# Optimization experiments

Measured on AMD Instinct MI355X. Metric: run time of the kernel, lower is better.

## Reference

```python
import jax, jax.numpy as jnp
import numpy as np

EPS = 1e-5
NUM_LAYERS = 3


def _batchnorm(h, g, b):
    mean = h.mean(axis=0)
    var = h.var(axis=0)  # biased variance, matches torch BatchNorm training math
    return (h - mean) * jax.lax.rsqrt(var + EPS) * g + b


def setup_inputs() -> dict:
    key = jax.random.key(0)
    ks = jax.random.split(key, 8)
    N, E, D, H, OUT = 100000, 1600000, 128, 128, 64
    s = 0.08  # weight scale for numerical sanity
    return {
        "x": jax.random.normal(ks[0], (N, D), jnp.float32),
        "edge_index": jax.random.randint(ks[1], (2, E), 0, N, jnp.int64),
        "Wl": jax.random.normal(ks[2], (NUM_LAYERS, D, H), jnp.float32) * s,
        "bl": jnp.zeros((NUM_LAYERS, H), jnp.float32),
        "Wr": jax.random.normal(ks[3], (NUM_LAYERS, D, H), jnp.float32) * s,
        "gamma": jnp.ones((NUM_LAYERS, H), jnp.float32),
        "beta": jnp.zeros((NUM_LAYERS, H), jnp.float32),
        "W1": jax.random.normal(ks[4], (D + NUM_LAYERS * H, 2 * OUT), jnp.float32) * s,
        "b1": jnp.zeros((2 * OUT,), jnp.float32),
        "g1": jnp.ones((2 * OUT,), jnp.float32),
        "be1": jnp.zeros((2 * OUT,), jnp.float32),
        "W2": jax.random.normal(ks[5], (2 * OUT, OUT), jnp.float32) * s,
        "b2": jnp.zeros((OUT,), jnp.float32),
    }


def reference(x, edge_index, Wl, bl, Wr, gamma, beta, W1, b1, g1, be1, W2, b2):
    # GraphSAGE: stacked SAGEConv(mean aggr) + BatchNorm + ReLU, JK-concat, 2-layer MLP head.
    # Dropout is identity (eval mode).
    N = x.shape[0]
    src, dst = edge_index[0], edge_index[1]
    deg = jax.ops.segment_sum(jnp.ones((src.shape[0],), x.dtype), dst, num_segments=N)
    inv_deg = (1.0 / jnp.maximum(deg, 1.0))[:, None]  # [N,1]
    xs = [x]
    h = x
    for i in range(NUM_LAYERS):
        # mean-aggregate neighbor features, then linear (same math as PyG SAGEConv)
        agg = jax.ops.segment_sum(h[src], dst, num_segments=N) * inv_deg  # [N,D]
        h = agg @ Wl[i] + bl[i] + h @ Wr[i]
        h = _batchnorm(h, gamma[i], beta[i])
        h = jax.nn.relu(h)
        xs.append(h)
    z = jnp.concatenate(xs, axis=-1)  # [N, D + L*H]
    z = _batchnorm(z @ W1 + b1, g1, be1)
    z = jax.nn.leaky_relu(z, negative_slope=0.01)
    return z @ W2 + b2
```

## Files before the change

kernel.cpp:

```cpp
#include <hip/hip_runtime.h>
#include <hip/hip_bf16.h>

#define CDIV(a,b) (((a)+(b)-1)/(b))

typedef __attribute__((ext_vector_type(8))) short short8_t;
typedef __attribute__((ext_vector_type(4))) float f32x4;

__device__ __forceinline__ float b2f(ushort u){
    union { uint i; float f; } v; v.i = ((uint)u) << 16; return v.f;
}
__device__ __forceinline__ ushort f2b(float f){
    __hip_bfloat16 h = __float2bfloat16(f);
    return *reinterpret_cast<ushort*>(&h);
}


__global__ __launch_bounds__(256) void k_bcount(
    const int* __restrict__ dst, int E, int nbuck, int* __restrict__ bcnt)
{
    __shared__ int cnt[512];
    const int t = threadIdx.x;
    for (int i = t; i < nbuck; i += 256) cnt[i] = 0;
    __syncthreads();
    const int e0 = blockIdx.x * 4096;
    #pragma unroll
    for (int q = 0; q < 16; ++q){
        int idx = e0 + q*256 + t;
        if (idx < E) atomicAdd(&cnt[dst[idx] >> 8], 1);
    }
    __syncthreads();
    for (int i = t; i < nbuck; i += 256){
        int c = cnt[i];
        if (c) atomicAdd(&bcnt[i], c);
    }
}

__global__ void k_bscan(const int* __restrict__ bcnt, int nbuck, int E,
                        int* __restrict__ bbase, int* __restrict__ gcur)
{
    __shared__ int s[512];
    int t = threadIdx.x;
    int v = (t < nbuck) ? bcnt[t] : 0;
    s[t] = v;
    __syncthreads();
    for (int off = 1; off < 512; off <<= 1){
        int x = (t >= off) ? s[t-off] : 0;
        __syncthreads();
        s[t] += x;
        __syncthreads();
    }
    if (t < nbuck){ int e = s[t] - v; bbase[t] = e; gcur[t] = e; }
    if (t == 0) bbase[nbuck] = E;
}

__global__ __launch_bounds__(256) void k_bucketA(
    const int* __restrict__ src, const int* __restrict__ dst, int E,
    int nbuck, int* __restrict__ gcur, uint* __restrict__ ebuf)
{
    __shared__ int cnt[512];
    __shared__ int base[512];
    const int t  = threadIdx.x;
    const int e0 = blockIdx.x * 4096;
    for (int i = t; i < nbuck; i += 256) cnt[i] = 0;
    __syncthreads();
    uint pk[16]; int mb[16];
    #pragma unroll
    for (int q = 0; q < 16; ++q){
        int idx = e0 + q*256 + t;
        int b = -1; uint pkv = 0;
        if (idx < E){
            int s = src[idx], d = dst[idx];
            b = d >> 8;
            pkv = (uint)s | ((uint)(d & 255) << 24);
            atomicAdd(&cnt[b], 1);
        }
        mb[q] = b; pk[q] = pkv;
    }
    __syncthreads();
    for (int i = t; i < nbuck; i += 256){
        int c = cnt[i];
        base[i] = c ? atomicAdd(&gcur[i], c) : 0;
    }
    __syncthreads();
    for (int i = t; i < nbuck; i += 256) cnt[i] = 0;
    __syncthreads();
    #pragma unroll
    for (int q = 0; q < 16; ++q){
        if (mb[q] >= 0){
            int b   = mb[q];
            int pos = base[b] + atomicAdd(&cnt[b], 1);
            ebuf[pos] = pk[q];
        }
    }
}

__global__ __launch_bounds__(256) void k_build(
    const uint* __restrict__ ebuf, const int* __restrict__ bbase,
    int N, int E, int* __restrict__ row_ptr, float* __restrict__ inv_deg,
    int* __restrict__ col_idx)
{
    __shared__ int cnt[256];
    __shared__ int scn[256];
    const int b = blockIdx.x;
    const int t = threadIdx.x;
    const int n0 = b << 8;
    const int ebase = bbase[b], eend = bbase[b+1];

    cnt[t] = 0;
    __syncthreads();
    for (int j = ebase + t; j < eend; j += 256)
        atomicAdd(&cnt[ebuf[j] >> 24], 1);
    __syncthreads();

    int d = cnt[t];
    scn[t] = d;
    __syncthreads();
    for (int off = 1; off < 256; off <<= 1){
        int x = (t >= off) ? scn[t-off] : 0;
        __syncthreads();
        scn[t] += x;
        __syncthreads();
    }
    int excl = scn[t] - d;
    int node = n0 + t;
    if (node < N){
        row_ptr[node] = ebase + excl;
        inv_deg[node] = 1.0f / (float)(d > 1 ? d : 1);
    }
    if (b == 0 && t == 0) row_ptr[N] = E;

    cnt[t] = excl;
    __syncthreads();
    for (int j = ebase + t; j < eend; j += 256){
        uint e = ebuf[j];
        int p = atomicAdd(&cnt[e >> 24], 1);
        col_idx[ebase + p] = (int)(e & 0xFFFFFFu);
    }
}

__global__ void k_cvt_x(const float* __restrict__ in, ushort* __restrict__ out, int n4){
    int i = blockIdx.x*blockDim.x + threadIdx.x;
    if (i >= n4) return;
    float4 v = reinterpret_cast<const float4*>(in)[i];
    ushort4 o; o.x=f2b(v.x); o.y=f2b(v.y); o.z=f2b(v.z); o.w=f2b(v.w);
    reinterpret_cast<ushort4*>(out)[i] = o;
}

__global__ void k_cvt_t(const float* __restrict__ in, ushort* __restrict__ out,
                        int K, int C, int total){
    int i = blockIdx.x*blockDim.x + threadIdx.x;
    if (i >= total) return;
    int kc = K*C;
    int s = i / kc, r = i - s*kc;
    int k = r / C, c = r - k*C;
    out[s*kc + c*K + k] = f2b(in[i]);
}

__global__ __launch_bounds__(256) void k_agg_bf(
    const ushort* __restrict__ h, const int* __restrict__ row_ptr,
    const int* __restrict__ col_idx, const float* __restrict__ inv_deg,
    ushort* __restrict__ agg, int N)
{
    int node = (blockIdx.x*blockDim.x + threadIdx.x) >> 6;
    int lane = threadIdx.x & 63;
    if (node >= N) return;
    const int g = lane >> 4, l15 = lane & 15;
    const int beg = row_ptr[node], end = row_ptr[node+1];

    float a[8];
    #pragma unroll
    for (int q = 0; q < 8; ++q) a[q] = 0.f;

    int j = beg + g;
    while (j + 4 < end){
        int s0 = col_idx[j];
        int s1 = col_idx[j+4];
        uint4 v0 = *reinterpret_cast<const uint4*>(h + (size_t)s0*128 + l15*8);
        uint4 v1 = *reinterpret_cast<const uint4*>(h + (size_t)s1*128 + l15*8);
        uint w0[4] = {v0.x, v0.y, v0.z, v0.w};
        uint w1[4] = {v1.x, v1.y, v1.z, v1.w};
        #pragma unroll
        for (int q = 0; q < 4; ++q){
            a[2*q]   += b2f((ushort)(w0[q] & 0xffffu)) + b2f((ushort)(w1[q] & 0xffffu));
            a[2*q+1] += b2f((ushort)(w0[q] >> 16))     + b2f((ushort)(w1[q] >> 16));
        }
        j += 8;
    }
    if (j < end){
        int s0 = col_idx[j];
        uint4 v0 = *reinterpret_cast<const uint4*>(h + (size_t)s0*128 + l15*8);
        uint w0[4] = {v0.x, v0.y, v0.z, v0.w};
        #pragma unroll
        for (int q = 0; q < 4; ++q){
            a[2*q]   += b2f((ushort)(w0[q] & 0xffffu));
            a[2*q+1] += b2f((ushort)(w0[q] >> 16));
        }
    }

    #pragma unroll
    for (int q = 0; q < 8; ++q){
        a[q] += __shfl_xor(a[q], 16);
        a[q] += __shfl_xor(a[q], 32);
    }

    if (g == 0){
        float sc = inv_deg[node];
        uint r[4];
        #pragma unroll
        for (int q = 0; q < 4; ++q)
            r[q] = (uint)f2b(a[2*q]*sc) | ((uint)f2b(a[2*q+1]*sc) << 16);
        *reinterpret_cast<uint4*>(agg + (size_t)node*128 + l15*8) =
            make_uint4(r[0], r[1], r[2], r[3]);
    }
}

template<int NCF, int STATS, int OUTBF>
__global__ __launch_bounds__(256) void k_gemm_mfma(
    const ushort* __restrict__ A0, const ushort* __restrict__ T0,
    const ushort* __restrict__ A1, const ushort* __restrict__ T1,
    const ushort* __restrict__ A2, const ushort* __restrict__ T2,
    const ushort* __restrict__ A3, const ushort* __restrict__ T3,
    int P, const float* __restrict__ bias,
    ushort* __restrict__ out_bf, float* __restrict__ out_f32,
    float* __restrict__ partials, int N)
{
    __shared__ ushort Ws[NCF*16*128];
    const int t   = threadIdx.x;
    const int w   = t >> 6, l = t & 63;
    const int l15 = l & 15, lg = l >> 4;
    const int r0   = blockIdx.x * 128;
    const int wrow = w * 32;

    f32x4 acc[2][NCF];
    #pragma unroll
    for (int i = 0; i < 2; ++i)
        #pragma unroll
        for (int j = 0; j < NCF; ++j) acc[i][j] = (f32x4){0.f,0.f,0.f,0.f};

    for (int p = 0; p < P; ++p){
        const ushort* A = (p==0)?A0:(p==1)?A1:(p==2)?A2:A3;
        const ushort* T = (p==0)?T0:(p==1)?T1:(p==2)?T2:T3;
        if (p) __syncthreads();
        #pragma unroll
        for (int q = 0; q < NCF; ++q){
            int lin  = q*256 + t;
            int row  = lin >> 4, c16 = lin & 15;
            int c16s = c16 ^ (row & 7);
            uint4 v = *reinterpret_cast<const uint4*>(T + (size_t)row*128 + c16*8);
            *reinterpret_cast<uint4*>(&Ws[row*128 + c16s*8]) = v;
        }
        __syncthreads();
        #pragma unroll
        for (int kk = 0; kk < 4; ++kk){
            const int k0 = kk*32;
            short8_t a[2];
            #pragma unroll
            for (int rf = 0; rf < 2; ++rf){
                size_t gr = (size_t)(r0 + wrow + rf*16 + l15);
                a[rf] = *reinterpret_cast<const short8_t*>(A + gr*128 + k0 + lg*8);
            }
            #pragma unroll
            for (int cf = 0; cf < NCF; ++cf){
                int row  = cf*16 + l15;
                int c16  = (k0 >> 3) + lg;
                int c16s = c16 ^ (row & 7);
                short8_t b = *reinterpret_cast<const short8_t*>(&Ws[row*128 + c16s*8]);
                acc[0][cf] = __builtin_amdgcn_mfma_f32_16x16x32_bf16(a[0], b, acc[0][cf], 0, 0, 0);
                acc[1][cf] = __builtin_amdgcn_mfma_f32_16x16x32_bf16(a[1], b, acc[1][cf], 0, 0, 0);
            }
        }
    }

    float bs[NCF];
    #pragma unroll
    for (int cf = 0; cf < NCF; ++cf) bs[cf] = bias[cf*16 + l15];

    float s1[NCF], s2[NCF];
    #pragma unroll
    for (int cf = 0; cf < NCF; ++cf){ s1[cf] = 0.f; s2[cf] = 0.f; }

    #pragma unroll
    for (int rf = 0; rf < 2; ++rf){
        #pragma unroll
        for (int q = 0; q < 4; ++q){
            int gr = r0 + wrow + rf*16 + lg*4 + q;
            bool valid = gr < N;
            #pragma unroll
            for (int cf = 0; cf < NCF; ++cf){
                float v = acc[rf][cf][q] + bs[cf];
                if (valid){
                    if (STATS){ s1[cf] += v; s2[cf] += v*v; }
                    int col = cf*16 + l15;
                    if (OUTBF) out_bf[(size_t)gr*(NCF*16) + col] = f2b(v);
                    else       out_f32[(size_t)gr*(NCF*16) + col] = v;
                }
            }
        }
    }
    if (STATS){
        #pragma unroll
        for (int cf = 0; cf < NCF; ++cf){
            s1[cf] += __shfl_xor(s1[cf], 16);
            s1[cf] += __shfl_xor(s1[cf], 32);
            s2[cf] += __shfl_xor(s2[cf], 16);
            s2[cf] += __shfl_xor(s2[cf], 32);
        }
        if (l < 16){
            float* pb = partials + (size_t)(blockIdx.x*4 + w)*256;
            #pragma unroll
            for (int cf = 0; cf < NCF; ++cf){
                pb[cf*16 + l15]       = s1[cf];
                pb[128 + cf*16 + l15] = s2[cf];
            }
        }
    }
}

__global__ void k_bnreduce(const float* __restrict__ partials, int I, int N,
                           const float* __restrict__ gamma, const float* __restrict__ beta,
                           float* __restrict__ ss)
{
    int c = blockIdx.x;
    int l = threadIdx.x;
    float s1 = 0.f, s2 = 0.f;
    for (int i = l; i < I; i += 64){
        s1 += partials[(size_t)i*256 + c];
        s2 += partials[(size_t)i*256 + 128 + c];
    }
    #pragma unroll
    for (int off = 32; off; off >>= 1){
        s1 += __shfl_xor(s1, off);
        s2 += __shfl_xor(s2, off);
    }
    if (l == 0){
        float m   = s1 / (float)N;
        float var = s2 / (float)N - m*m;
        float sc  = rsqrtf(var + 1e-5f) * gamma[c];
        ss[c]     = sc;
        ss[128+c] = beta[c] - m*sc;
    }
}

template<int LEAKY>
__global__ __launch_bounds__(256) void k_norm_act_bf(
    const ushort* __restrict__ pre, const float* __restrict__ ss,
    ushort* __restrict__ out, int total8)
{
    int i = blockIdx.x*blockDim.x + threadIdx.x;
    if (i >= total8) return;
    uint4 v = reinterpret_cast<const uint4*>(pre)[i];
    int c0 = (i & 15) * 8;
    uint vv[4] = {v.x, v.y, v.z, v.w};
    uint r[4];
    #pragma unroll
    for (int q = 0; q < 4; ++q){
        float f0 = b2f((ushort)(vv[q] & 0xffffu)) * ss[c0+q*2]   + ss[128+c0+q*2];
        float f1 = b2f((ushort)(vv[q] >> 16))     * ss[c0+q*2+1] + ss[128+c0+q*2+1];
        if (LEAKY){ f0 = f0 > 0.f ? f0 : 0.01f*f0; f1 = f1 > 0.f ? f1 : 0.01f*f1; }
        else      { f0 = fmaxf(f0, 0.f); f1 = fmaxf(f1, 0.f); }
        r[q] = (uint)f2b(f0) | ((uint)f2b(f1) << 16);
    }
    reinterpret_cast<uint4*>(out)[i] = make_uint4(r[0], r[1], r[2], r[3]);
}

extern "C" void kernel_launch(void* const* d_in, const int* in_sizes, int n_in,
                              void* d_out, int out_size, void* d_ws, size_t ws_size,
                              hipStream_t stream)
{
    const float* x     = (const float*)d_in[0];
    const int*   ei    = (const int*)  d_in[1];
    const float* Wl    = (const float*)d_in[2];
    const float* bl    = (const float*)d_in[3];
    const float* Wr    = (const float*)d_in[4];
    const float* gamma = (const float*)d_in[5];
    const float* beta  = (const float*)d_in[6];
    const float* W1    = (const float*)d_in[7];
    const float* b1    = (const float*)d_in[8];
    const float* g1    = (const float*)d_in[9];
    const float* be1   = (const float*)d_in[10];
    const float* W2    = (const float*)d_in[11];
    const float* b2    = (const float*)d_in[12];
    float* out = (float*)d_out;

    const int N  = in_sizes[0] / 128;
    const int E  = in_sizes[1] / 2;
    const int NB = CDIV(N, 128);
    const size_t NPAD = (size_t)NB * 128;
    const int* src = ei;
    const int* dst = ei + E;

    const int NBUCK = CDIV(N, 256);

    char* w = (char*)d_ws;
    const size_t SB = NPAD * 128 * sizeof(ushort);
    ushort* x_bf = (ushort*)(w + 0*SB);
    ushort* h0   = (ushort*)(w + 1*SB);
    ushort* h1   = (ushort*)(w + 2*SB);
    ushort* h2   = (ushort*)(w + 3*SB);
    ushort* aggb = (ushort*)(w + 4*SB);
    ushort* preb = (ushort*)(w + 5*SB);
    char* p = w + 6*SB;
    ushort* WtL = (ushort*)p;  p += (size_t)3*16384*2;
    ushort* WtR = (ushort*)p;  p += (size_t)3*16384*2;
    ushort* Wt1 = (ushort*)p;  p += (size_t)4*16384*2;
    ushort* Wt2 = (ushort*)p;  p += (size_t)8192*2;
    float* partials = (float*)p; p += (size_t)NB*4*256*sizeof(float);
    uint*  ebuf     = (uint*)p;  p += (size_t)E*4;
    int*   col_idx  = (int*)p;   p += (size_t)E*4;
    int*   row_ptr  = (int*)p;   p += (size_t)(N+1)*4;
    float* inv_deg  = (float*)p; p += (size_t)N*4;
    int*   bcnt     = (int*)p;   p += 512*4;
    int*   bbase    = (int*)p;   p += 516*4;
    int*   gcur     = (int*)p;   p += 512*4;
    float* ssb      = (float*)p; p += 256*4;

    const int n4 = N * 32;
    k_cvt_x<<<CDIV(n4,256), 256, 0, stream>>>(x, x_bf, n4);
    k_cvt_t<<<CDIV(3*16384,256), 256, 0, stream>>>(Wl, WtL, 128, 128, 3*16384);
    k_cvt_t<<<CDIV(3*16384,256), 256, 0, stream>>>(Wr, WtR, 128, 128, 3*16384);
    k_cvt_t<<<CDIV(4*16384,256), 256, 0, stream>>>(W1, Wt1, 128, 128, 4*16384);
    k_cvt_t<<<CDIV(8192,256),    256, 0, stream>>>(W2, Wt2, 128,  64, 8192);

    hipMemsetAsync(bcnt, 0, 512*4, stream);
    k_bcount<<<CDIV(E,4096), 256, 0, stream>>>(dst, E, NBUCK, bcnt);
    k_bscan<<<1, 512, 0, stream>>>(bcnt, NBUCK, E, bbase, gcur);
    k_bucketA<<<CDIV(E,4096), 256, 0, stream>>>(src, dst, E, NBUCK, gcur, ebuf);
    k_build<<<NBUCK, 256, 0, stream>>>(ebuf, bbase, N, E, row_ptr, inv_deg, col_idx);

    const ushort* h = x_bf;
    ushort* hb[3] = {h0, h1, h2};
    const int total8 = N * 16;
    for (int L = 0; L < 3; ++L){
        k_agg_bf<<<CDIV(N,4), 256, 0, stream>>>(h, row_ptr, col_idx, inv_deg, aggb, N);
        k_gemm_mfma<8,1,1><<<NB, 256, 0, stream>>>(
            aggb, WtL + (size_t)L*16384,
            h,    WtR + (size_t)L*16384,
            nullptr, nullptr, nullptr, nullptr,
            2, bl + (size_t)L*128, preb, nullptr, partials, N);
        k_bnreduce<<<128, 64, 0, stream>>>(partials, NB*4, N,
            gamma + (size_t)L*128, beta + (size_t)L*128, ssb);
        k_norm_act_bf<0><<<CDIV(total8,256), 256, 0, stream>>>(preb, ssb, hb[L], total8);
        h = hb[L];
    }

    k_gemm_mfma<8,1,1><<<NB, 256, 0, stream>>>(
        x_bf, Wt1 + 0,
        h0,   Wt1 + 16384,
        h1,   Wt1 + 2*16384,
        h2,   Wt1 + 3*16384,
        4, b1, preb, nullptr, partials, N);
    k_bnreduce<<<128, 64, 0, stream>>>(partials, NB*4, N, g1, be1, ssb);
    k_norm_act_bf<1><<<CDIV(total8,256), 256, 0, stream>>>(preb, ssb, aggb, total8);

    k_gemm_mfma<4,0,0><<<NB, 256, 0, stream>>>(
        aggb, Wt2, nullptr, nullptr, nullptr, nullptr, nullptr, nullptr,
        1, b2, nullptr, out, nullptr, N);
}
```

Baseline: 521.2 us.

## Fuse GEMM, batchnorm reduce and activation via cooperative grid sync; unroll aggregation

```diff
diff --git a/kernel.cpp b/kernel.cpp
--- a/kernel.cpp
+++ b/kernel.cpp
@@ -1,5 +1,8 @@
 #include <hip/hip_runtime.h>
 #include <hip/hip_bf16.h>
+#include <hip/hip_cooperative_groups.h>
+
+namespace cg = cooperative_groups;
 
 #define CDIV(a,b) (((a)+(b)-1)/(b))
 
@@ -13,7 +16,6 @@
     __hip_bfloat16 h = __float2bfloat16(f);
     return *reinterpret_cast<ushort*>(&h);
 }
-
 
 __global__ __launch_bounds__(256) void k_bcount(
     const int* __restrict__ dst, int E, int nbuck, int* __restrict__ bcnt)
@@ -156,6 +158,18 @@
     out[s*kc + c*K + k] = f2b(in[i]);
 }
 
+__device__ __forceinline__ void acc8(float2* a, uint4 v){
+    uint w[4] = {v.x, v.y, v.z, v.w};
+    #pragma unroll
+    for (int q = 0; q < 4; ++q){
+        union { uint i; float f; } lo, hi;
+        lo.i = w[q] << 16;
+        hi.i = w[q] & 0xffff0000u;
+        a[q].x += lo.f;
+        a[q].y += hi.f;
+    }
+}
+
 __global__ __launch_bounds__(256) void k_agg_bf(
     const ushort* __restrict__ h, const int* __restrict__ row_ptr,
     const int* __restrict__ col_idx, const float* __restrict__ inv_deg,
@@ -166,41 +180,33 @@
     if (node >= N) return;
     const int g = lane >> 4, l15 = lane & 15;
     const int beg = row_ptr[node], end = row_ptr[node+1];
-
-    float a[8];
-    #pragma unroll
-    for (int q = 0; q < 8; ++q) a[q] = 0.f;
+    const size_t co = (size_t)l15 * 8;
+
+    float2 a2[4];
+    #pragma unroll
+    for (int q = 0; q < 4; ++q) a2[q] = make_float2(0.f, 0.f);
 
     int j = beg + g;
-    while (j + 4 < end){
-        int s0 = col_idx[j];
-        int s1 = col_idx[j+4];
-        uint4 v0 = *reinterpret_cast<const uint4*>(h + (size_t)s0*128 + l15*8);
-        uint4 v1 = *reinterpret_cast<const uint4*>(h + (size_t)s1*128 + l15*8);
-        uint w0[4] = {v0.x, v0.y, v0.z, v0.w};
-        uint w1[4] = {v1.x, v1.y, v1.z, v1.w};
-        #pragma unroll
-        for (int q = 0; q < 4; ++q){
-            a[2*q]   += b2f((ushort)(w0[q] & 0xffffu)) + b2f((ushort)(w1[q] & 0xffffu));
-            a[2*q+1] += b2f((ushort)(w0[q] >> 16))     + b2f((ushort)(w1[q] >> 16));
-        }
-        j += 8;
-    }
-    if (j < end){
-        int s0 = col_idx[j];
-        uint4 v0 = *reinterpret_cast<const uint4*>(h + (size_t)s0*128 + l15*8);
-        uint w0[4] = {v0.x, v0.y, v0.z, v0.w};
-        #pragma unroll
-        for (int q = 0; q < 4; ++q){
-            a[2*q]   += b2f((ushort)(w0[q] & 0xffffu));
-            a[2*q+1] += b2f((ushort)(w0[q] >> 16));
-        }
-    }
-
-    #pragma unroll
-    for (int q = 0; q < 8; ++q){
-        a[q] += __shfl_xor(a[q], 16);
-        a[q] += __shfl_xor(a[q], 32);
+    for (; j + 12 < end; j += 16){
+        int i0 = col_idx[j], i1 = col_idx[j+4], i2 = col_idx[j+8], i3 = col_idx[j+12];
+        uint4 v0 = *reinterpret_cast<const uint4*>(h + (size_t)i0*128 + co);
+        uint4 v1 = *reinterpret_cast<const uint4*>(h + (size_t)i1*128 + co);
+        uint4 v2 = *reinterpret_cast<const uint4*>(h + (size_t)i2*128 + co);
+        uint4 v3 = *reinterpret_cast<const uint4*>(h + (size_t)i3*128 + co);
+        acc8(a2, v0); acc8(a2, v1); acc8(a2, v2); acc8(a2, v3);
+    }
+    for (; j < end; j += 4){
+        int i0 = col_idx[j];
+        uint4 v0 = *reinterpret_cast<const uint4*>(h + (size_t)i0*128 + co);
+        acc8(a2, v0);
+    }
+
+    #pragma unroll
+    for (int q = 0; q < 4; ++q){
+        a2[q].x += __shfl_xor(a2[q].x, 16);
+        a2[q].y += __shfl_xor(a2[q].y, 16);
+        a2[q].x += __shfl_xor(a2[q].x, 32);
+        a2[q].y += __shfl_xor(a2[q].y, 32);
     }
 
     if (g == 0){
@@ -208,9 +214,155 @@
         uint r[4];
         #pragma unroll
         for (int q = 0; q < 4; ++q)
-            r[q] = (uint)f2b(a[2*q]*sc) | ((uint)f2b(a[2*q+1]*sc) << 16);
-        *reinterpret_cast<uint4*>(agg + (size_t)node*128 + l15*8) =
+            r[q] = (uint)f2b(a2[q].x*sc) | ((uint)f2b(a2[q].y*sc) << 16);
+        *reinterpret_cast<uint4*>(agg + (size_t)node*128 + co) =
             make_uint4(r[0], r[1], r[2], r[3]);
+    }
+}
+
+template<int LEAKY>
+__global__ __launch_bounds__(256, 4) void k_gemm_fused(
+    const ushort* __restrict__ A0, const ushort* __restrict__ T0,
+    const ushort* __restrict__ A1, const ushort* __restrict__ T1,
+    const ushort* __restrict__ A2, const ushort* __restrict__ T2,
+    const ushort* __restrict__ A3, const ushort* __restrict__ T3,
+    int P, const float* __restrict__ bias,
+    const float* __restrict__ gamma, const float* __restrict__ beta,
+    ushort* __restrict__ hout, float* __restrict__ partials,
+    float* __restrict__ ss, int N, int NB)
+{
+    __shared__ ushort Ws[8*16*128];
+    __shared__ float red[512];
+    const int t   = threadIdx.x;
+    const int w   = t >> 6, l = t & 63;
+    const int l15 = l & 15, lg = l >> 4;
+    const int r0   = blockIdx.x * 128;
+    const int wrow = w * 32;
+
+    f32x4 acc[2][8];
+    #pragma unroll
+    for (int i = 0; i < 2; ++i)
+        #pragma unroll
+        for (int j = 0; j < 8; ++j) acc[i][j] = (f32x4){0.f,0.f,0.f,0.f};
+
+    for (int p = 0; p < P; ++p){
+        const ushort* A = (p==0)?A0:(p==1)?A1:(p==2)?A2:A3;
+        const ushort* T = (p==0)?T0:(p==1)?T1:(p==2)?T2:T3;
+        if (p) __syncthreads();
+        #pragma unroll
+        for (int q = 0; q < 8; ++q){
+            int lin  = q*256 + t;
+            int row  = lin >> 4, c16 = lin & 15;
+            int c16s = c16 ^ (row & 7);
+            uint4 v = *reinterpret_cast<const uint4*>(T + (size_t)row*128 + c16*8);
+            *reinterpret_cast<uint4*>(&Ws[row*128 + c16s*8]) = v;
+        }
+        __syncthreads();
+        #pragma unroll
+        for (int kk = 0; kk < 4; ++kk){
+            const int k0 = kk*32;
+            short8_t a[2];
+            #pragma unroll
+            for (int rf = 0; rf < 2; ++rf){
+                size_t gr = (size_t)(r0 + wrow + rf*16 + l15);
+                a[rf] = *reinterpret_cast<const short8_t*>(A + gr*128 + k0 + lg*8);
+            }
+            #pragma unroll
+            for (int cf = 0; cf < 8; ++cf){
+                int row  = cf*16 + l15;
+                int c16  = (k0 >> 3) + lg;
+                int c16s = c16 ^ (row & 7);
+                short8_t b = *reinterpret_cast<const short8_t*>(&Ws[row*128 + c16s*8]);
+                acc[0][cf] = __builtin_amdgcn_mfma_f32_16x16x32_bf16(a[0], b, acc[0][cf], 0, 0, 0);
+                acc[1][cf] = __builtin_amdgcn_mfma_f32_16x16x32_bf16(a[1], b, acc[1][cf], 0, 0, 0);
+            }
+        }
+    }
+
+    float bs[8];
+    #pragma unroll
+    for (int cf = 0; cf < 8; ++cf) bs[cf] = bias[cf*16 + l15];
+
+    float s1[8], s2[8];
+    #pragma unroll
+    for (int cf = 0; cf < 8; ++cf){ s1[cf] = 0.f; s2[cf] = 0.f; }
+    #pragma unroll
+    for (int rf = 0; rf < 2; ++rf){
+        #pragma unroll
+        for (int q = 0; q < 4; ++q){
+            int gr = r0 + wrow + rf*16 + lg*4 + q;
+            bool valid = gr < N;
+            #pragma unroll
+            for (int cf = 0; cf < 8; ++cf){
+                float v = acc[rf][cf][q] + bs[cf];
+                if (valid){ s1[cf] += v; s2[cf] += v*v; }
+            }
+        }
+    }
+    #pragma unroll
+    for (int cf = 0; cf < 8; ++cf){
+        s1[cf] += __shfl_xor(s1[cf], 16);
+        s1[cf] += __shfl_xor(s1[cf], 32);
+        s2[cf] += __shfl_xor(s2[cf], 16);
+        s2[cf] += __shfl_xor(s2[cf], 32);
+    }
+    if (l < 16){
+        float* pb = partials + (size_t)(blockIdx.x*4 + w)*256;
+        #pragma unroll
+        for (int cf = 0; cf < 8; ++cf){
+            pb[cf*16 + l15]       = s1[cf];
+            pb[128 + cf*16 + l15] = s2[cf];
+        }
+    }
+
+    cg::this_grid().sync();
+
+    if (blockIdx.x < 128){
+        int c = blockIdx.x;
+        int I = NB * 4;
+        float r1 = 0.f, r2 = 0.f;
+        for (int i = t; i < I; i += 256){
+            r1 += partials[(size_t)i*256 + c];
+            r2 += partials[(size_t)i*256 + 128 + c];
+        }
+        red[t] = r1; red[256+t] = r2;
+        __syncthreads();
+        for (int off = 128; off; off >>= 1){
+            if (t < off){ red[t] += red[t+off]; red[256+t] += red[256+t+off]; }
+            __syncthreads();
+        }
+        if (t == 0){
+            float m   = red[0] / (float)N;
+            float var = red[256] / (float)N - m*m;
+            float scv = rsqrtf(var + 1e-5f) * gamma[c];
+            ss[c]     = scv;
+            ss[128+c] = beta[c] - m*scv;
+        }
+    }
+
+    cg::this_grid().sync();
+
+    float sc[8], sh[8];
+    #pragma unroll
+    for (int cf = 0; cf < 8; ++cf){
+        sc[cf] = ss[cf*16 + l15];
+        sh[cf] = ss[128 + cf*16 + l15];
+    }
+    #pragma unroll
+    for (int rf = 0; rf < 2; ++rf){
+        #pragma unroll
+        for (int q = 0; q < 4; ++q){
+            int gr = r0 + wrow + rf*16 + lg*4 + q;
+            if (gr < N){
+                #pragma unroll
+                for (int cf = 0; cf < 8; ++cf){
+                    float v = (acc[rf][cf][q] + bs[cf]) * sc[cf] + sh[cf];
+                    if (LEAKY) v = v > 0.f ? v : 0.01f*v;
+                    else       v = fmaxf(v, 0.f);
+                    hout[(size_t)gr*128 + cf*16 + l15] = f2b(v);
+                }
+            }
+        }
     }
 }
 
@@ -427,30 +579,43 @@
     k_bucketA<<<CDIV(E,4096), 256, 0, stream>>>(src, dst, E, NBUCK, gcur, ebuf);
     k_build<<<NBUCK, 256, 0, stream>>>(ebuf, bbase, N, E, row_ptr, inv_deg, col_idx);
 
+    int Nv = N, NBv = NB;
+    const int total8 = N * 16;
+
+    auto fused = [&](const ushort* A0, const ushort* T0, const ushort* A1, const ushort* T1,
+                     const ushort* A2, const ushort* T2, const ushort* A3, const ushort* T3,
+                     int P, const float* bias, const float* gm, const float* bt,
+                     ushort* hout, int leaky) -> bool {
+        void* args[] = {&A0,&T0,&A1,&T1,&A2,&T2,&A3,&T3,&P,&bias,&gm,&bt,
+                        &hout,&partials,&ssb,&Nv,&NBv};
+        const void* fn = leaky ? (const void*)k_gemm_fused<1> : (const void*)k_gemm_fused<0>;
+        if (hipLaunchCooperativeKernel(fn, dim3(NB), dim3(256), args, 0, stream) == hipSuccess)
+            return true;
+        k_gemm_mfma<8,1,1><<<NB, 256, 0, stream>>>(A0,T0,A1,T1,A2,T2,A3,T3,P,bias,
+                                                   preb, nullptr, partials, N);
+        k_bnreduce<<<128, 64, 0, stream>>>(partials, NB*4, N, gm, bt, ssb);
+        if (leaky) k_norm_act_bf<1><<<CDIV(total8,256), 256, 0, stream>>>(preb, ssb, hout, total8);
+        else       k_norm_act_bf<0><<<CDIV(total8,256), 256, 0, stream>>>(preb, ssb, hout, total8);
+        return false;
+    };
+
     const ushort* h = x_bf;
     ushort* hb[3] = {h0, h1, h2};
-    const int total8 = N * 16;
     for (int L = 0; L < 3; ++L){
         k_agg_bf<<<CDIV(N,4), 256, 0, stream>>>(h, row_ptr, col_idx, inv_deg, aggb, N);
-        k_gemm_mfma<8,1,1><<<NB, 256, 0, stream>>>(
-            aggb, WtL + (size_t)L*16384,
-            h,    WtR + (size_t)L*16384,
-            nullptr, nullptr, nullptr, nullptr,
-            2, bl + (size_t)L*128, preb, nullptr, partials, N);
-        k_bnreduce<<<128, 64, 0, stream>>>(partials, NB*4, N,
-            gamma + (size_t)L*128, beta + (size_t)L*128, ssb);
-        k_norm_act_bf<0><<<CDIV(total8,256), 256, 0, stream>>>(preb, ssb, hb[L], total8);
+        fused(aggb, WtL + (size_t)L*16384,
+              h,    WtR + (size_t)L*16384,
+              nullptr, nullptr, nullptr, nullptr,
+              2, bl + (size_t)L*128, gamma + (size_t)L*128, beta + (size_t)L*128,
+              hb[L], 0);
         h = hb[L];
     }
 
-    k_gemm_mfma<8,1,1><<<NB, 256, 0, stream>>>(
-        x_bf, Wt1 + 0,
-        h0,   Wt1 + 16384,
-        h1,   Wt1 + 2*16384,
-        h2,   Wt1 + 3*16384,
-        4, b1, preb, nullptr, partials, N);
-    k_bnreduce<<<128, 64, 0, stream>>>(partials, NB*4, N, g1, be1, ssb);
-    k_norm_act_bf<1><<<CDIV(total8,256), 256, 0, stream>>>(preb, ssb, aggb, total8);
+    fused(x_bf, Wt1 + 0,
+          h0,   Wt1 + 16384,
+          h1,   Wt1 + 2*16384,
+          h2,   Wt1 + 3*16384,
+          4, b1, g1, be1, aggb, 1);
 
     k_gemm_mfma<4,0,0><<<NB, 256, 0, stream>>>(
         aggb, Wt2, nullptr, nullptr, nullptr, nullptr, nullptr, nullptr,
```

New measurement: 1.074 ms. 2.06x slower.

## Fuse BatchNorm+activation into consumer aggregation and GEMM operand loads

Applied to the files above, without the earlier changes.

```diff
diff --git a/kernel.cpp b/kernel.cpp
--- a/kernel.cpp
+++ b/kernel.cpp
@@ -13,7 +13,6 @@
     __hip_bfloat16 h = __float2bfloat16(f);
     return *reinterpret_cast<ushort*>(&h);
 }
-
 
 __global__ __launch_bounds__(256) void k_bcount(
     const int* __restrict__ dst, int E, int nbuck, int* __restrict__ bcnt)
@@ -156,51 +155,73 @@
     out[s*kc + c*K + k] = f2b(in[i]);
 }
 
+template<int NORM>
 __global__ __launch_bounds__(256) void k_agg_bf(
     const ushort* __restrict__ h, const int* __restrict__ row_ptr,
     const int* __restrict__ col_idx, const float* __restrict__ inv_deg,
-    ushort* __restrict__ agg, int N)
+    const float* __restrict__ ssp, ushort* __restrict__ agg, int N)
 {
     int node = (blockIdx.x*blockDim.x + threadIdx.x) >> 6;
     int lane = threadIdx.x & 63;
     if (node >= N) return;
     const int g = lane >> 4, l15 = lane & 15;
     const int beg = row_ptr[node], end = row_ptr[node+1];
-
-    float a[8];
-    #pragma unroll
-    for (int q = 0; q < 8; ++q) a[q] = 0.f;
+    const size_t co = (size_t)l15 * 8;
+
+    float scv[8], shv[8];
+    if (NORM){
+        float4 c0 = *reinterpret_cast<const float4*>(ssp + co);
+        float4 c1 = *reinterpret_cast<const float4*>(ssp + co + 4);
+        float4 s0 = *reinterpret_cast<const float4*>(ssp + 128 + co);
+        float4 s1 = *reinterpret_cast<const float4*>(ssp + 128 + co + 4);
+        scv[0]=c0.x; scv[1]=c0.y; scv[2]=c0.z; scv[3]=c0.w;
+        scv[4]=c1.x; scv[5]=c1.y; scv[6]=c1.z; scv[7]=c1.w;
+        shv[0]=s0.x; shv[1]=s0.y; shv[2]=s0.z; shv[3]=s0.w;
+        shv[4]=s1.x; shv[5]=s1.y; shv[6]=s1.z; shv[7]=s1.w;
+    }
+
+    float2 a2[4];
+    #pragma unroll
+    for (int q = 0; q < 4; ++q) a2[q] = make_float2(0.f, 0.f);
+
+    auto acc8 = [&](uint4 v){
+        uint w[4] = {v.x, v.y, v.z, v.w};
+        #pragma unroll
+        for (int q = 0; q < 4; ++q){
+            union { uint i; float f; } lo, hi;
+            lo.i = w[q] << 16;
+            hi.i = w[q] & 0xffff0000u;
+            float fl = lo.f, fh = hi.f;
+            if (NORM){
+                fl = fmaxf(fl*scv[2*q]   + shv[2*q],   0.f);
+                fh = fmaxf(fh*scv[2*q+1] + shv[2*q+1], 0.f);
+            }
+            a2[q].x += fl;
+            a2[q].y += fh;
+        }
+    };
 
     int j = beg + g;
-    while (j + 4 < end){
-        int s0 = col_idx[j];
-        int s1 = col_idx[j+4];
-        uint4 v0 = *reinterpret_cast<const uint4*>(h + (size_t)s0*128 + l15*8);
-        uint4 v1 = *reinterpret_cast<const uint4*>(h + (size_t)s1*128 + l15*8);
-        uint w0[4] = {v0.x, v0.y, v0.z, v0.w};
-        uint w1[4] = {v1.x, v1.y, v1.z, v1.w};
-        #pragma unroll
-        for (int q = 0; q < 4; ++q){
-            a[2*q]   += b2f((ushort)(w0[q] & 0xffffu)) + b2f((ushort)(w1[q] & 0xffffu));
-            a[2*q+1] += b2f((ushort)(w0[q] >> 16))     + b2f((ushort)(w1[q] >> 16));
-        }
-        j += 8;
-    }
-    if (j < end){
-        int s0 = col_idx[j];
-        uint4 v0 = *reinterpret_cast<const uint4*>(h + (size_t)s0*128 + l15*8);
-        uint w0[4] = {v0.x, v0.y, v0.z, v0.w};
-        #pragma unroll
-        for (int q = 0; q < 4; ++q){
-            a[2*q]   += b2f((ushort)(w0[q] & 0xffffu));
-            a[2*q+1] += b2f((ushort)(w0[q] >> 16));
-        }
-    }
-
-    #pragma unroll
-    for (int q = 0; q < 8; ++q){
-        a[q] += __shfl_xor(a[q], 16);
-        a[q] += __shfl_xor(a[q], 32);
+    for (; j + 12 < end; j += 16){
+        int i0 = col_idx[j], i1 = col_idx[j+4], i2 = col_idx[j+8], i3 = col_idx[j+12];
+        uint4 v0 = *reinterpret_cast<const uint4*>(h + (size_t)i0*128 + co);
+        uint4 v1 = *reinterpret_cast<const uint4*>(h + (size_t)i1*128 + co);
+        uint4 v2 = *reinterpret_cast<const uint4*>(h + (size_t)i2*128 + co);
+        uint4 v3 = *reinterpret_cast<const uint4*>(h + (size_t)i3*128 + co);
+        acc8(v0); acc8(v1); acc8(v2); acc8(v3);
+    }
+    for (; j < end; j += 4){
+        int i0 = col_idx[j];
+        uint4 v0 = *reinterpret_cast<const uint4*>(h + (size_t)i0*128 + co);
+        acc8(v0);
+    }
+
+    #pragma unroll
+    for (int q = 0; q < 4; ++q){
+        a2[q].x += __shfl_xor(a2[q].x, 16);
+        a2[q].y += __shfl_xor(a2[q].y, 16);
+        a2[q].x += __shfl_xor(a2[q].x, 32);
+        a2[q].y += __shfl_xor(a2[q].y, 32);
     }
 
     if (g == 0){
@@ -208,10 +229,35 @@
         uint r[4];
         #pragma unroll
         for (int q = 0; q < 4; ++q)
-            r[q] = (uint)f2b(a[2*q]*sc) | ((uint)f2b(a[2*q+1]*sc) << 16);
-        *reinterpret_cast<uint4*>(agg + (size_t)node*128 + l15*8) =
+            r[q] = (uint)f2b(a2[q].x*sc) | ((uint)f2b(a2[q].y*sc) << 16);
+        *reinterpret_cast<uint4*>(agg + (size_t)node*128 + co) =
             make_uint4(r[0], r[1], r[2], r[3]);
     }
+}
+
+__device__ __forceinline__ short8_t norm_frag(short8_t a, const float* __restrict__ sp,
+                                              int kbase, int leaky)
+{
+    float4 c0 = *reinterpret_cast<const float4*>(sp + kbase);
+    float4 c1 = *reinterpret_cast<const float4*>(sp + kbase + 4);
+    float4 h0 = *reinterpret_cast<const float4*>(sp + 128 + kbase);
+    float4 h1 = *reinterpret_cast<const float4*>(sp + 128 + kbase + 4);
+    float cs[8] = {c0.x,c0.y,c0.z,c0.w,c1.x,c1.y,c1.z,c1.w};
+    float hs[8] = {h0.x,h0.y,h0.z,h0.w,h1.x,h1.y,h1.z,h1.w};
+    uint* au = reinterpret_cast<uint*>(&a);
+    short8_t r;
+    uint* ru = reinterpret_cast<uint*>(&r);
+    #pragma unroll
+    for (int q = 0; q < 4; ++q){
+        float lo = b2f((ushort)(au[q] & 0xffffu));
+        float hi = b2f((ushort)(au[q] >> 16));
+        lo = lo*cs[2*q]   + hs[2*q];
+        hi = hi*cs[2*q+1] + hs[2*q+1];
+        if (leaky){ lo = lo > 0.f ? lo : 0.01f*lo; hi = hi > 0.f ? hi : 0.01f*hi; }
+        else      { lo = fmaxf(lo, 0.f); hi = fmaxf(hi, 0.f); }
+        ru[q] = (uint)f2b(lo) | ((uint)f2b(hi) << 16);
+    }
+    return r;
 }
 
 template<int NCF, int STATS, int OUTBF>
@@ -220,6 +266,9 @@
     const ushort* __restrict__ A1, const ushort* __restrict__ T1,
     const ushort* __restrict__ A2, const ushort* __restrict__ T2,
     const ushort* __restrict__ A3, const ushort* __restrict__ T3,
+    const float* __restrict__ ns0, const float* __restrict__ ns1,
+    const float* __restrict__ ns2, const float* __restrict__ ns3,
+    int m0, int m1, int m2, int m3,
     int P, const float* __restrict__ bias,
     ushort* __restrict__ out_bf, float* __restrict__ out_f32,
     float* __restrict__ partials, int N)
@@ -238,8 +287,10 @@
         for (int j = 0; j < NCF; ++j) acc[i][j] = (f32x4){0.f,0.f,0.f,0.f};
 
     for (int p = 0; p < P; ++p){
-        const ushort* A = (p==0)?A0:(p==1)?A1:(p==2)?A2:A3;
-        const ushort* T = (p==0)?T0:(p==1)?T1:(p==2)?T2:T3;
+        const ushort* A  = (p==0)?A0:(p==1)?A1:(p==2)?A2:A3;
+        const ushort* T  = (p==0)?T0:(p==1)?T1:(p==2)?T2:T3;
+        const float*  ns = (p==0)?ns0:(p==1)?ns1:(p==2)?ns2:ns3;
+        const int     md = (p==0)?m0:(p==1)?m1:(p==2)?m2:m3;
         if (p) __syncthreads();
         #pragma unroll
         for (int q = 0; q < NCF; ++q){
@@ -258,6 +309,10 @@
             for (int rf = 0; rf < 2; ++rf){
                 size_t gr = (size_t)(r0 + wrow + rf*16 + l15);
                 a[rf] = *reinterpret_cast<const short8_t*>(A + gr*128 + k0 + lg*8);
+            }
+            if (md){
+                a[0] = norm_frag(a[0], ns, k0 + lg*8, md == 2);
+                a[1] = norm_frag(a[1], ns, k0 + lg*8, md == 2);
             }
             #pragma unroll
             for (int cf = 0; cf < NCF; ++cf){
@@ -339,28 +394,6 @@
         ss[c]     = sc;
         ss[128+c] = beta[c] - m*sc;
     }
-}
-
-template<int LEAKY>
-__global__ __launch_bounds__(256) void k_norm_act_bf(
-    const ushort* __restrict__ pre, const float* __restrict__ ss,
-    ushort* __restrict__ out, int total8)
-{
-    int i = blockIdx.x*blockDim.x + threadIdx.x;
-    if (i >= total8) return;
-    uint4 v = reinterpret_cast<const uint4*>(pre)[i];
-    int c0 = (i & 15) * 8;
-    uint vv[4] = {v.x, v.y, v.z, v.w};
-    uint r[4];
-    #pragma unroll
-    for (int q = 0; q < 4; ++q){
-        float f0 = b2f((ushort)(vv[q] & 0xffffu)) * ss[c0+q*2]   + ss[128+c0+q*2];
-        float f1 = b2f((ushort)(vv[q] >> 16))     * ss[c0+q*2+1] + ss[128+c0+q*2+1];
-        if (LEAKY){ f0 = f0 > 0.f ? f0 : 0.01f*f0; f1 = f1 > 0.f ? f1 : 0.01f*f1; }
-        else      { f0 = fmaxf(f0, 0.f); f1 = fmaxf(f1, 0.f); }
-        r[q] = (uint)f2b(f0) | ((uint)f2b(f1) << 16);
-    }
-    reinterpret_cast<uint4*>(out)[i] = make_uint4(r[0], r[1], r[2], r[3]);
 }
 
 extern "C" void kernel_launch(void* const* d_in, const int* in_sizes, int n_in,
@@ -394,11 +427,11 @@
     char* w = (char*)d_ws;
     const size_t SB = NPAD * 128 * sizeof(ushort);
     ushort* x_bf = (ushort*)(w + 0*SB);
-    ushort* h0   = (ushort*)(w + 1*SB);
-    ushort* h1   = (ushort*)(w + 2*SB);
-    ushort* h2   = (ushort*)(w + 3*SB);
+    ushort* pre0 = (ushort*)(w + 1*SB);
+    ushort* pre1 = (ushort*)(w + 2*SB);
+    ushort* pre2 = (ushort*)(w + 3*SB);
     ushort* aggb = (ushort*)(w + 4*SB);
-    ushort* preb = (ushort*)(w + 5*SB);
+    ushort* preh = (ushort*)(w + 5*SB);
     char* p = w + 6*SB;
     ushort* WtL = (ushort*)p;  p += (size_t)3*16384*2;
     ushort* WtR = (ushort*)p;  p += (size_t)3*16384*2;
@@ -412,7 +445,10 @@
     int*   bcnt     = (int*)p;   p += 512*4;
     int*   bbase    = (int*)p;   p += 516*4;
     int*   gcur     = (int*)p;   p += 512*4;
-    float* ssb      = (float*)p; p += 256*4;
+    float* ss0      = (float*)p; p += 256*4;
+    float* ss1      = (float*)p; p += 256*4;
+    float* ss2      = (float*)p; p += 256*4;
+    float* ssh      = (float*)p; p += 256*4;
 
     const int n4 = N * 32;
     k_cvt_x<<<CDIV(n4,256), 256, 0, stream>>>(x, x_bf, n4);
@@ -427,32 +463,44 @@
     k_bucketA<<<CDIV(E,4096), 256, 0, stream>>>(src, dst, E, NBUCK, gcur, ebuf);
     k_build<<<NBUCK, 256, 0, stream>>>(ebuf, bbase, N, E, row_ptr, inv_deg, col_idx);
 
-    const ushort* h = x_bf;
-    ushort* hb[3] = {h0, h1, h2};
-    const int total8 = N * 16;
+    ushort* pre[3] = {pre0, pre1, pre2};
+    float*  ssl[3] = {ss0, ss1, ss2};
+    const int I = NB * 4;
+
     for (int L = 0; L < 3; ++L){
-        k_agg_bf<<<CDIV(N,4), 256, 0, stream>>>(h, row_ptr, col_idx, inv_deg, aggb, N);
+        if (L == 0)
+            k_agg_bf<0><<<CDIV(N,4), 256, 0, stream>>>(x_bf, row_ptr, col_idx, inv_deg,
+                                                       nullptr, aggb, N);
+        else
+            k_agg_bf<1><<<CDIV(N,4), 256, 0, stream>>>(pre[L-1], row_ptr, col_idx, inv_deg,
+                                                       ssl[L-1], aggb, N);
+        const ushort* hsrc = (L == 0) ? x_bf : pre[L-1];
+        const float*  hns  = (L == 0) ? nullptr : ssl[L-1];
+        int hmode = (L == 0) ? 0 : 1;
         k_gemm_mfma<8,1,1><<<NB, 256, 0, stream>>>(
             aggb, WtL + (size_t)L*16384,
-            h,    WtR + (size_t)L*16384,
+            hsrc, WtR + (size_t)L*16384,
             nullptr, nullptr, nullptr, nullptr,
-            2, bl + (size_t)L*128, preb, nullptr, partials, N);
-        k_bnreduce<<<128, 64, 0, stream>>>(partials, NB*4, N,
-            gamma + (size_t)L*128, beta + (size_t)L*128, ssb);
-        k_norm_act_bf<0><<<CDIV(total8,256), 256, 0, stream>>>(preb, ssb, hb[L], total8);
-        h = hb[L];
+            nullptr, hns, nullptr, nullptr,
+            0, hmode, 0, 0,
+            2, bl + (size_t)L*128, pre[L], nullptr, partials, N);
+        k_bnreduce<<<128, 64, 0, stream>>>(partials, I, N,
+            gamma + (size_t)L*128, beta + (size_t)L*128, ssl[L]);
     }
 
     k_gemm_mfma<8,1,1><<<NB, 256, 0, stream>>>(
         x_bf, Wt1 + 0,
-        h0,   Wt1 + 16384,
-        h1,   Wt1 + 2*16384,
-        h2,   Wt1 + 3*16384,
-        4, b1, preb, nullptr, partials, N);
-    k_bnreduce<<<128, 64, 0, stream>>>(partials, NB*4, N, g1, be1, ssb);
-    k_norm_act_bf<1><<<CDIV(total8,256), 256, 0, stream>>>(preb, ssb, aggb, total8);
+        pre0, Wt1 + 16384,
+        pre1, Wt1 + 2*16384,
+        pre2, Wt1 + 3*16384,
+        nullptr, ss0, ss1, ss2,
+        0, 1, 1, 1,
+        4, b1, preh, nullptr, partials, N);
+    k_bnreduce<<<128, 64, 0, stream>>>(partials, I, N, g1, be1, ssh);
 
     k_gemm_mfma<4,0,0><<<NB, 256, 0, stream>>>(
-        aggb, Wt2, nullptr, nullptr, nullptr, nullptr, nullptr, nullptr,
-        1, b2, nullptr, out, nullptr, N);
-}
+        preh, Wt2, nullptr, nullptr, nullptr, nullptr, nullptr, nullptr,
+        ssh, nullptr, nullptr, nullptr,
+        2, 0, 0, 0,
+        1, b2, nullptr, out, partials, N);
+}
```

After: 517.4 us. About the same (-0.7%).
